# Kernel tuning notes

Measured on AMD Instinct MI355X. Metric: run time of the kernel, lower is better.

## Reference

```python
import jax, jax.numpy as jnp
import numpy as np

E, T, A, H = 64, 128, 32, 4
S, O, QH1, QD, C1 = 256, 128, 128, 64, 128  # state, obs, query hidden, query/key dim, c hidden


def setup_inputs() -> dict:
    key = jax.random.key(0)
    ks = jax.random.split(key, 10)
    w = 0.02
    return {
        "q_values": jax.random.normal(ks[0], (E, T, A), jnp.float32),
        "states": jax.random.normal(ks[1], (E, T, S), jnp.float32),
        "individual_fs": jax.random.normal(ks[2], (E, T, A, O), jnp.float32),
        "Wq1": jax.random.normal(ks[3], (S, QH1), jnp.float32) * w,
        "bq1": jnp.zeros((QH1,), jnp.float32),
        "Wq2": jax.random.normal(ks[4], (QH1, QD), jnp.float32) * w,
        "bq2": jnp.zeros((QD,), jnp.float32),
        "Wk": jax.random.normal(ks[5], (H, O, QD), jnp.float32) * w,
        "bk": jnp.zeros((H, QD), jnp.float32),
        "Wc1": jax.random.normal(ks[6], (S, C1), jnp.float32) * w,
        "bc1": jnp.zeros((C1,), jnp.float32),
        "Wc2": jax.random.normal(ks[7], (C1, 1), jnp.float32) * w,
        "bc2": jnp.zeros((1,), jnp.float32),
    }


def reference(q_values, states, individual_fs, Wq1, bq1, Wq2, bq2, Wk, bk, Wc1, bc1, Wc2, bc2):
    e, t, a = q_values.shape
    s = states.reshape(-1, states.shape[-1])              # (B, S), B = E*T
    f = individual_fs.reshape(e * t, a, -1)               # (B, A, O)
    # query embedding of state: 2-layer MLP with ReLU
    emb_s = jnp.maximum(s @ Wq1 + bq1, 0.0) @ Wq2 + bq2   # (B, QD)
    # all-agents, all-heads key extraction in one batched einsum
    emb_u = jnp.einsum('bao,hok->bahk', f, Wk) + bk       # (B, A, H, QD)
    # query-key dot products per agent/head, then sum over heads
    Lambda_i = jnp.einsum('bk,bahk->bah', emb_s, emb_u).sum(axis=-1)  # (B, A)
    # state-dependent scalar bias
    c_value = jnp.maximum(s @ Wc1 + bc1, 0.0) @ Wc2 + bc2  # (B, 1)
    Q_tot = jnp.sum(Lambda_i * q_values.reshape(-1, a), axis=-1, keepdims=True) + c_value
    return Q_tot.reshape(e, t, 1)
```

## Files before the change

### kernel.cpp

```cpp
#include <hip/hip_runtime.h>


static constexpr int Sd  = 256;
static constexpr int Ad  = 32;
static constexpr int Od  = 128;
static constexpr int QDd = 64;
static constexpr int NB  = 8;

__global__ void qatten_prep(const float* __restrict__ Wk, const float* __restrict__ bk,
                            float* __restrict__ WkT, float* __restrict__ bkSum)
{
    int idx = blockIdx.x * 256 + threadIdx.x;
    int k = idx >> 7;
    int o = idx & 127;
    float s = 0.f;
#pragma unroll
    for (int h = 0; h < 4; ++h) s += Wk[h * (Od * QDd) + o * QDd + k];
    WkT[k * Od + o] = s;
    if (idx < QDd) {
        float t = 0.f;
#pragma unroll
        for (int h = 0; h < 4; ++h) t += bk[h * QDd + idx];
        bkSum[idx] = t;
    }
}

__global__ __launch_bounds__(256, 4) void qatten_fused(
    const float* __restrict__ qv, const float* __restrict__ st, const float* __restrict__ fs,
    const float* __restrict__ Wq1, const float* __restrict__ bq1,
    const float* __restrict__ Wq2, const float* __restrict__ bq2,
    const float* __restrict__ Wc1, const float* __restrict__ bc1,
    const float* __restrict__ Wc2, const float* __restrict__ bc2,
    const float* __restrict__ WkT, const float* __restrict__ bkSum,
    float* __restrict__ out)
{
    __shared__ float s_lds[NB][Sd];
    __shared__ float h_lds[NB][260];
    __shared__ float emb_lds[NB][QDd];
    __shared__ float v_lds[NB][Od];
    __shared__ float q_lds[NB][Ad];
    __shared__ float red_lds[NB][4];
    __shared__ float bias_lds[NB];

    const int tid = threadIdx.x;
    const int b0 = blockIdx.x * NB;

    {
        const float4* sp = (const float4*)(st + (size_t)b0 * Sd);
        float4* sl = (float4*)&s_lds[0][0];
        sl[tid] = sp[tid];
        sl[tid + 256] = sp[tid + 256];
        (&q_lds[0][0])[tid] = qv[(size_t)b0 * Ad + tid];
    }
    __syncthreads();

    {
        const float* W  = (tid < 128) ? (Wq1 + tid) : (Wc1 + (tid - 128));
        const float  bb = (tid < 128) ? bq1[tid] : bc1[tid - 128];
        float acc[NB];
#pragma unroll
        for (int r = 0; r < NB; ++r) acc[r] = 0.f;
#pragma unroll 4
        for (int i = 0; i < Sd; i += 4) {
            const float w0 = W[(size_t)(i + 0) * 128];
            const float w1 = W[(size_t)(i + 1) * 128];
            const float w2 = W[(size_t)(i + 2) * 128];
            const float w3 = W[(size_t)(i + 3) * 128];
#pragma unroll
            for (int r = 0; r < NB; ++r) {
                const float4 sv = *(const float4*)&s_lds[r][i];
                float a = acc[r];
                a = fmaf(sv.x, w0, a);
                a = fmaf(sv.y, w1, a);
                a = fmaf(sv.z, w2, a);
                a = fmaf(sv.w, w3, a);
                acc[r] = a;
            }
        }
#pragma unroll
        for (int r = 0; r < NB; ++r)
            h_lds[r][tid] = fmaxf(acc[r] + bb, 0.f);
    }
    __syncthreads();

    {
        const int k = tid & 63;
        const int rg = tid >> 6;
        float a0 = 0.f, a1 = 0.f;
#pragma unroll 4
        for (int j = 0; j < 128; j += 4) {
            const float w0 = Wq2[(size_t)(j + 0) * 64 + k];
            const float w1 = Wq2[(size_t)(j + 1) * 64 + k];
            const float w2 = Wq2[(size_t)(j + 2) * 64 + k];
            const float w3 = Wq2[(size_t)(j + 3) * 64 + k];
            const float4 h0 = *(const float4*)&h_lds[rg][j];
            const float4 h1 = *(const float4*)&h_lds[rg + 4][j];
            a0 = fmaf(h0.x, w0, a0);  a1 = fmaf(h1.x, w0, a1);
            a0 = fmaf(h0.y, w1, a0);  a1 = fmaf(h1.y, w1, a1);
            a0 = fmaf(h0.z, w2, a0);  a1 = fmaf(h1.z, w2, a1);
            a0 = fmaf(h0.w, w3, a0);  a1 = fmaf(h1.w, w3, a1);
        }
        const float bias = bq2[k];
        emb_lds[rg][k] = a0 + bias;
        emb_lds[rg + 4][k] = a1 + bias;
    }
    __syncthreads();

    {
        const int o = tid & 127;
        const int rg = (tid >> 7) * 4;
        float acc[4] = {0.f, 0.f, 0.f, 0.f};
#pragma unroll 4
        for (int k = 0; k < QDd; k += 4) {
            const float w0 = WkT[(size_t)(k + 0) * 128 + o];
            const float w1 = WkT[(size_t)(k + 1) * 128 + o];
            const float w2 = WkT[(size_t)(k + 2) * 128 + o];
            const float w3 = WkT[(size_t)(k + 3) * 128 + o];
#pragma unroll
            for (int r = 0; r < 4; ++r) {
                const float4 ev = *(const float4*)&emb_lds[rg + r][k];
                float a = acc[r];
                a = fmaf(ev.x, w0, a);
                a = fmaf(ev.y, w1, a);
                a = fmaf(ev.z, w2, a);
                a = fmaf(ev.w, w3, a);
                acc[r] = a;
            }
        }
#pragma unroll
        for (int r = 0; r < 4; ++r) v_lds[rg + r][o] = acc[r];
    }

    {
        const int b = tid >> 5;
        const int i = tid & 31;
        float pb = 0.f, pc = 0.f;
#pragma unroll
        for (int k = i; k < QDd; k += 32)  pb = fmaf(emb_lds[b][k], bkSum[k], pb);
#pragma unroll
        for (int j = i; j < 128; j += 32)  pc = fmaf(h_lds[b][128 + j], Wc2[j], pc);
        float pq = q_lds[b][i];
#pragma unroll
        for (int d = 16; d >= 1; d >>= 1) {
            pb += __shfl_down(pb, d, 32);
            pc += __shfl_down(pc, d, 32);
            pq += __shfl_down(pq, d, 32);
        }
        if (i == 0) bias_lds[b] = (pc + bc2[0]) + pb * pq;
    }
    __syncthreads();

    {
        const int oq = tid & 31;
        const int ag = tid >> 5;
        float acc[NB];
#pragma unroll
        for (int b = 0; b < NB; ++b) {
            const float4* fb = (const float4*)(fs + (size_t)(b0 + b) * (Ad * Od));
            const float4 v4 = *(const float4*)&v_lds[b][oq * 4];
            float s = 0.f;
#pragma unroll
            for (int r = 0; r < 4; ++r) {
                const int a = ag + 8 * r;
                const float4 f4 = fb[a * 32 + oq];
                float d = f4.x * v4.x;
                d = fmaf(f4.y, v4.y, d);
                d = fmaf(f4.z, v4.z, d);
                d = fmaf(f4.w, v4.w, d);
                s = fmaf(q_lds[b][a], d, s);
            }
            acc[b] = s;
        }
        const int lane = tid & 63;
        const int wv = tid >> 6;
#pragma unroll
        for (int b = 0; b < NB; ++b) {
            float s = acc[b];
#pragma unroll
            for (int d = 32; d >= 1; d >>= 1) s += __shfl_xor(s, d);
            acc[b] = s;
        }
        if (lane == 0) {
#pragma unroll
            for (int b = 0; b < NB; ++b) red_lds[b][wv] = acc[b];
        }
    }
    __syncthreads();

    if (tid < NB) {
        out[b0 + tid] = red_lds[tid][0] + red_lds[tid][1] +
                        red_lds[tid][2] + red_lds[tid][3] + bias_lds[tid];
    }
}

extern "C" void kernel_launch(void* const* d_in, const int* in_sizes, int n_in,
                              void* d_out, int out_size, void* d_ws, size_t ws_size,
                              hipStream_t stream) {
    const float* qv  = (const float*)d_in[0];
    const float* st  = (const float*)d_in[1];
    const float* fs  = (const float*)d_in[2];
    const float* Wq1 = (const float*)d_in[3];
    const float* bq1 = (const float*)d_in[4];
    const float* Wq2 = (const float*)d_in[5];
    const float* bq2 = (const float*)d_in[6];
    const float* Wk  = (const float*)d_in[7];
    const float* bk  = (const float*)d_in[8];
    const float* Wc1 = (const float*)d_in[9];
    const float* bc1 = (const float*)d_in[10];
    const float* Wc2 = (const float*)d_in[11];
    const float* bc2 = (const float*)d_in[12];
    float* out = (float*)d_out;

    float* WkT   = (float*)d_ws;
    float* bkSum = WkT + QDd * Od;

    qatten_prep<<<32, 256, 0, stream>>>(Wk, bk, WkT, bkSum);
    qatten_fused<<<1024, 256, 0, stream>>>(qv, st, fs, Wq1, bq1, Wq2, bq2,
                                           Wc1, bc1, Wc2, bc2, WkT, bkSum, out);
}
```

Before: 246.6 us.

## Fold Wq2 into key weights and split MLP from feature streaming kernel

Precomputes M = Wq2·sum_h Wk (and the matching bias terms) in a second prep kernel, so the per-row work skips the 64-dim embedding layer and goes straight from the hidden layer to the 128-dim key-space vector. The fused kernel is split in two. One MLP kernel processes 16 rows per block and writes v and the bias to the workspace. A separate streaming kernel then reads the large individual_fs tensor with one wave per row at higher occupancy. This adds two extra launches and a round trip through global memory for v and the bias, in exchange for less arithmetic and better bandwidth use on the dominant fs read.

```diff
diff --git a/kernel.cpp b/kernel.cpp
--- a/kernel.cpp
+++ b/kernel.cpp
@@ -5,10 +5,18 @@
 static constexpr int Ad  = 32;
 static constexpr int Od  = 128;
 static constexpr int QDd = 64;
-static constexpr int NB  = 8;
-
-__global__ void qatten_prep(const float* __restrict__ Wk, const float* __restrict__ bk,
-                            float* __restrict__ WkT, float* __restrict__ bkSum)
+
+static constexpr size_t WS_WKT   = 0;
+static constexpr size_t WS_BKSUM = 8192;
+static constexpr size_t WS_M     = 8256;
+static constexpr size_t WS_V0    = 24640;
+static constexpr size_t WS_MBETA = 24768;
+static constexpr size_t WS_BETA0 = 24896;
+static constexpr size_t WS_BIAS  = 24960;
+static constexpr size_t WS_V     = 33216;
+
+__global__ void qatten_prep1(const float* __restrict__ Wk, const float* __restrict__ bk,
+                             float* __restrict__ WkT, float* __restrict__ bkSum)
 {
     int idx = blockIdx.x * 256 + threadIdx.x;
     int k = idx >> 7;
@@ -25,49 +33,77 @@
     }
 }
 
-__global__ __launch_bounds__(256, 4) void qatten_fused(
-    const float* __restrict__ qv, const float* __restrict__ st, const float* __restrict__ fs,
+__global__ void qatten_prep2(const float* __restrict__ Wq2, const float* __restrict__ bq2,
+                             const float* __restrict__ WkT, const float* __restrict__ bkSum,
+                             float* __restrict__ M, float* __restrict__ v0,
+                             float* __restrict__ m_beta, float* __restrict__ beta0)
+{
+    int idx = blockIdx.x * 256 + threadIdx.x;
+    int j = idx >> 7;
+    int o = idx & 127;
+    float acc = 0.f;
+    for (int k = 0; k < QDd; ++k)
+        acc = fmaf(Wq2[j * QDd + k], WkT[k * Od + o], acc);
+    M[j * Od + o] = acc;
+    if (idx < 128) {
+        float a = 0.f;
+        for (int k = 0; k < QDd; ++k) a = fmaf(bq2[k], WkT[k * Od + idx], a);
+        v0[idx] = a;
+    } else if (idx < 256) {
+        const int jj = idx - 128;
+        float a = 0.f;
+        for (int k = 0; k < QDd; ++k) a = fmaf(Wq2[jj * QDd + k], bkSum[k], a);
+        m_beta[jj] = a;
+    }
+    if (idx == 0) {
+        float a = 0.f;
+        for (int k = 0; k < QDd; ++k) a = fmaf(bq2[k], bkSum[k], a);
+        beta0[0] = a;
+    }
+}
+
+static constexpr int NBM = 16;
+
+__global__ __launch_bounds__(256, 4) void qatten_mlp(
+    const float* __restrict__ qv, const float* __restrict__ st,
     const float* __restrict__ Wq1, const float* __restrict__ bq1,
-    const float* __restrict__ Wq2, const float* __restrict__ bq2,
     const float* __restrict__ Wc1, const float* __restrict__ bc1,
     const float* __restrict__ Wc2, const float* __restrict__ bc2,
-    const float* __restrict__ WkT, const float* __restrict__ bkSum,
-    float* __restrict__ out)
-{
-    __shared__ float s_lds[NB][Sd];
-    __shared__ float h_lds[NB][260];
-    __shared__ float emb_lds[NB][QDd];
-    __shared__ float v_lds[NB][Od];
-    __shared__ float q_lds[NB][Ad];
-    __shared__ float red_lds[NB][4];
-    __shared__ float bias_lds[NB];
+    const float* __restrict__ M, const float* __restrict__ v0,
+    const float* __restrict__ m_beta, const float* __restrict__ beta0p,
+    float* __restrict__ v_ws, float* __restrict__ bias_ws)
+{
+    __shared__ float s_lds[NBM][Sd];
+    __shared__ float h_lds[NBM][258];
+    __shared__ float q_lds[NBM][Ad];
 
     const int tid = threadIdx.x;
-    const int b0 = blockIdx.x * NB;
+    const int b0 = blockIdx.x * NBM;
 
     {
         const float4* sp = (const float4*)(st + (size_t)b0 * Sd);
         float4* sl = (float4*)&s_lds[0][0];
-        sl[tid] = sp[tid];
-        sl[tid + 256] = sp[tid + 256];
-        (&q_lds[0][0])[tid] = qv[(size_t)b0 * Ad + tid];
+#pragma unroll
+        for (int i = 0; i < 4; ++i) sl[tid + i * 256] = sp[tid + i * 256];
+        float* ql = &q_lds[0][0];
+#pragma unroll
+        for (int i = 0; i < 2; ++i) ql[tid + i * 256] = qv[(size_t)b0 * Ad + tid + i * 256];
     }
     __syncthreads();
 
     {
         const float* W  = (tid < 128) ? (Wq1 + tid) : (Wc1 + (tid - 128));
         const float  bb = (tid < 128) ? bq1[tid] : bc1[tid - 128];
-        float acc[NB];
-#pragma unroll
-        for (int r = 0; r < NB; ++r) acc[r] = 0.f;
-#pragma unroll 4
+        float acc[NBM];
+#pragma unroll
+        for (int r = 0; r < NBM; ++r) acc[r] = 0.f;
         for (int i = 0; i < Sd; i += 4) {
             const float w0 = W[(size_t)(i + 0) * 128];
             const float w1 = W[(size_t)(i + 1) * 128];
             const float w2 = W[(size_t)(i + 2) * 128];
             const float w3 = W[(size_t)(i + 3) * 128];
 #pragma unroll
-            for (int r = 0; r < NB; ++r) {
+            for (int r = 0; r < NBM; ++r) {
                 const float4 sv = *(const float4*)&s_lds[r][i];
                 float a = acc[r];
                 a = fmaf(sv.x, w0, a);
@@ -78,119 +114,88 @@
             }
         }
 #pragma unroll
-        for (int r = 0; r < NB; ++r)
+        for (int r = 0; r < NBM; ++r)
             h_lds[r][tid] = fmaxf(acc[r] + bb, 0.f);
     }
     __syncthreads();
 
     {
-        const int k = tid & 63;
-        const int rg = tid >> 6;
-        float a0 = 0.f, a1 = 0.f;
-#pragma unroll 4
+        const int o = tid & 127;
+        const int rg = (tid >> 7) * 8;
+        float acc[8];
+#pragma unroll
+        for (int r = 0; r < 8; ++r) acc[r] = 0.f;
         for (int j = 0; j < 128; j += 4) {
-            const float w0 = Wq2[(size_t)(j + 0) * 64 + k];
-            const float w1 = Wq2[(size_t)(j + 1) * 64 + k];
-            const float w2 = Wq2[(size_t)(j + 2) * 64 + k];
-            const float w3 = Wq2[(size_t)(j + 3) * 64 + k];
-            const float4 h0 = *(const float4*)&h_lds[rg][j];
-            const float4 h1 = *(const float4*)&h_lds[rg + 4][j];
-            a0 = fmaf(h0.x, w0, a0);  a1 = fmaf(h1.x, w0, a1);
-            a0 = fmaf(h0.y, w1, a0);  a1 = fmaf(h1.y, w1, a1);
-            a0 = fmaf(h0.z, w2, a0);  a1 = fmaf(h1.z, w2, a1);
-            a0 = fmaf(h0.w, w3, a0);  a1 = fmaf(h1.w, w3, a1);
-        }
-        const float bias = bq2[k];
-        emb_lds[rg][k] = a0 + bias;
-        emb_lds[rg + 4][k] = a1 + bias;
-    }
-    __syncthreads();
-
-    {
-        const int o = tid & 127;
-        const int rg = (tid >> 7) * 4;
-        float acc[4] = {0.f, 0.f, 0.f, 0.f};
-#pragma unroll 4
-        for (int k = 0; k < QDd; k += 4) {
-            const float w0 = WkT[(size_t)(k + 0) * 128 + o];
-            const float w1 = WkT[(size_t)(k + 1) * 128 + o];
-            const float w2 = WkT[(size_t)(k + 2) * 128 + o];
-            const float w3 = WkT[(size_t)(k + 3) * 128 + o];
-#pragma unroll
-            for (int r = 0; r < 4; ++r) {
-                const float4 ev = *(const float4*)&emb_lds[rg + r][k];
+            const float m0 = M[(size_t)(j + 0) * 128 + o];
+            const float m1 = M[(size_t)(j + 1) * 128 + o];
+            const float m2 = M[(size_t)(j + 2) * 128 + o];
+            const float m3 = M[(size_t)(j + 3) * 128 + o];
+#pragma unroll
+            for (int r = 0; r < 8; ++r) {
+                const float4 hv = *(const float4*)&h_lds[rg + r][j];
                 float a = acc[r];
-                a = fmaf(ev.x, w0, a);
-                a = fmaf(ev.y, w1, a);
-                a = fmaf(ev.z, w2, a);
-                a = fmaf(ev.w, w3, a);
+                a = fmaf(hv.x, m0, a);
+                a = fmaf(hv.y, m1, a);
+                a = fmaf(hv.z, m2, a);
+                a = fmaf(hv.w, m3, a);
                 acc[r] = a;
             }
         }
-#pragma unroll
-        for (int r = 0; r < 4; ++r) v_lds[rg + r][o] = acc[r];
-    }
-
-    {
-        const int b = tid >> 5;
-        const int i = tid & 31;
+        const float v0o = v0[o];
+#pragma unroll
+        for (int r = 0; r < 8; ++r)
+            v_ws[(size_t)(b0 + rg + r) * 128 + o] = acc[r] + v0o;
+    }
+
+    {
+        const int b = tid >> 4;
+        const int i = tid & 15;
         float pb = 0.f, pc = 0.f;
 #pragma unroll
-        for (int k = i; k < QDd; k += 32)  pb = fmaf(emb_lds[b][k], bkSum[k], pb);
-#pragma unroll
-        for (int j = i; j < 128; j += 32)  pc = fmaf(h_lds[b][128 + j], Wc2[j], pc);
-        float pq = q_lds[b][i];
-#pragma unroll
-        for (int d = 16; d >= 1; d >>= 1) {
-            pb += __shfl_down(pb, d, 32);
-            pc += __shfl_down(pc, d, 32);
-            pq += __shfl_down(pq, d, 32);
-        }
-        if (i == 0) bias_lds[b] = (pc + bc2[0]) + pb * pq;
-    }
-    __syncthreads();
-
-    {
-        const int oq = tid & 31;
-        const int ag = tid >> 5;
-        float acc[NB];
-#pragma unroll
-        for (int b = 0; b < NB; ++b) {
-            const float4* fb = (const float4*)(fs + (size_t)(b0 + b) * (Ad * Od));
-            const float4 v4 = *(const float4*)&v_lds[b][oq * 4];
-            float s = 0.f;
-#pragma unroll
-            for (int r = 0; r < 4; ++r) {
-                const int a = ag + 8 * r;
-                const float4 f4 = fb[a * 32 + oq];
-                float d = f4.x * v4.x;
-                d = fmaf(f4.y, v4.y, d);
-                d = fmaf(f4.z, v4.z, d);
-                d = fmaf(f4.w, v4.w, d);
-                s = fmaf(q_lds[b][a], d, s);
-            }
-            acc[b] = s;
-        }
-        const int lane = tid & 63;
-        const int wv = tid >> 6;
-#pragma unroll
-        for (int b = 0; b < NB; ++b) {
-            float s = acc[b];
-#pragma unroll
-            for (int d = 32; d >= 1; d >>= 1) s += __shfl_xor(s, d);
-            acc[b] = s;
-        }
-        if (lane == 0) {
-#pragma unroll
-            for (int b = 0; b < NB; ++b) red_lds[b][wv] = acc[b];
-        }
-    }
-    __syncthreads();
-
-    if (tid < NB) {
-        out[b0 + tid] = red_lds[tid][0] + red_lds[tid][1] +
-                        red_lds[tid][2] + red_lds[tid][3] + bias_lds[tid];
-    }
+        for (int t = 0; t < 8; ++t) {
+            const int j = i + 16 * t;
+            pb = fmaf(h_lds[b][j], m_beta[j], pb);
+            pc = fmaf(h_lds[b][128 + j], Wc2[j], pc);
+        }
+        float pq = q_lds[b][i] + q_lds[b][i + 16];
+#pragma unroll
+        for (int d = 8; d >= 1; d >>= 1) {
+            pb += __shfl_down(pb, d, 16);
+            pc += __shfl_down(pc, d, 16);
+            pq += __shfl_down(pq, d, 16);
+        }
+        if (i == 0) bias_ws[b0 + b] = (pc + bc2[0]) + (pb + beta0p[0]) * pq;
+    }
+}
+
+__global__ __launch_bounds__(256, 8) void qatten_stream(
+    const float* __restrict__ qv, const float* __restrict__ fs,
+    const float* __restrict__ v_ws, const float* __restrict__ bias_ws,
+    float* __restrict__ out)
+{
+    const int gw   = (blockIdx.x * 256 + threadIdx.x) >> 6;
+    const int lane = threadIdx.x & 63;
+    const int oq   = lane & 31;
+    const int a0   = lane >> 5;
+
+    const float4* fb = (const float4*)(fs + (size_t)gw * (Ad * Od));
+    const float4  v4 = *(const float4*)(v_ws + (size_t)gw * Od + oq * 4);
+    const float*  qb = qv + (size_t)gw * Ad;
+
+    float s = 0.f;
+#pragma unroll
+    for (int r = 0; r < 16; ++r) {
+        const int a = a0 + 2 * r;
+        const float4 f4 = fb[a * 32 + oq];
+        float d = f4.x * v4.x;
+        d = fmaf(f4.y, v4.y, d);
+        d = fmaf(f4.z, v4.z, d);
+        d = fmaf(f4.w, v4.w, d);
+        s = fmaf(qb[a], d, s);
+    }
+#pragma unroll
+    for (int d = 32; d >= 1; d >>= 1) s += __shfl_xor(s, d);
+    if (lane == 0) out[gw] = s + bias_ws[gw];
 }
 
 extern "C" void kernel_launch(void* const* d_in, const int* in_sizes, int n_in,
@@ -211,10 +216,19 @@
     const float* bc2 = (const float*)d_in[12];
     float* out = (float*)d_out;
 
-    float* WkT   = (float*)d_ws;
-    float* bkSum = WkT + QDd * Od;
-
-    qatten_prep<<<32, 256, 0, stream>>>(Wk, bk, WkT, bkSum);
-    qatten_fused<<<1024, 256, 0, stream>>>(qv, st, fs, Wq1, bq1, Wq2, bq2,
-                                           Wc1, bc1, Wc2, bc2, WkT, bkSum, out);
-}
+    float* ws      = (float*)d_ws;
+    float* WkT     = ws + WS_WKT;
+    float* bkSum   = ws + WS_BKSUM;
+    float* Mm      = ws + WS_M;
+    float* v0      = ws + WS_V0;
+    float* m_beta  = ws + WS_MBETA;
+    float* beta0   = ws + WS_BETA0;
+    float* bias_ws = ws + WS_BIAS;
+    float* v_ws    = ws + WS_V;
+
+    qatten_prep1<<<32, 256, 0, stream>>>(Wk, bk, WkT, bkSum);
+    qatten_prep2<<<64, 256, 0, stream>>>(Wq2, bq2, WkT, bkSum, Mm, v0, m_beta, beta0);
+    qatten_mlp<<<512, 256, 0, stream>>>(qv, st, Wq1, bq1, Wc1, bc1, Wc2, bc2,
+                                        Mm, v0, m_beta, beta0, v_ws, bias_ws);
+    qatten_stream<<<2048, 256, 0, stream>>>(qv, fs, v_ws, bias_ws, out);
+}
```

Result: slower. 268.7 us (+9.0%).
